# Optimization experiments

Hardware: AMD Instinct MI355X
Metric: run time of the kernel (lower is better)

Reference implementation:

```python
import jax, jax.numpy as jnp
import numpy as np

B, T, E, UNITS, VOCAB, NCLS = 128, 512, 256, 256, 50257, 2

def setup_inputs() -> dict:
    key = jax.random.key(0)
    ks = jax.random.split(key, 7)
    s = 0.05
    return {
        "sentence": jax.random.randint(ks[0], (B, T), 0, VOCAB, dtype=jnp.int32),
        "emb_table": jax.random.normal(ks[1], (VOCAB, E), jnp.float32) * s,
        "W": jax.random.normal(ks[2], (1, UNITS, E), jnp.float32) * s,
        "U": jax.random.normal(ks[3], (1, UNITS, UNITS), jnp.float32) * s,
        "W1": jax.random.normal(ks[4], (UNITS, 32), jnp.float32) * s,
        "b1": jnp.zeros((32,), jnp.float32),
        "W2": jax.random.normal(ks[5], (32, NCLS), jnp.float32) * s,
        "b2": jnp.zeros((NCLS,), jnp.float32),
    }

def reference(sentence, emb_table, W, U, W1, b1, W2, b2):
    # Embedding lookup: [B, T, E]
    emb = emb_table[sentence]
    # Precompute input projection for all timesteps in one batched GEMM:
    # x @ W[0].T for every t -> [T, B, units]
    xW = jnp.einsum('bte,ue->tbu', emb, W[0])
    Ut = U[0].T  # [units, units]

    def step(h, xw_t):
        h_new = jnp.tanh(xw_t + h @ Ut)
        return h_new, None

    h0 = jnp.zeros((sentence.shape[0], W.shape[1]), emb.dtype)
    h_final, _ = jax.lax.scan(step, h0, xW)

    # Classification head (dropout is identity at inference)
    hidden = jax.nn.relu(h_final @ W1 + b1)
    logits = hidden @ W2 + b2
    return jax.nn.softmax(logits, axis=-1)
```

## Files before the change

kernel.cpp:

```cpp
#include <hip/hip_runtime.h>
#include <stdint.h>

#define TT 512
#define NB 128
#define EM 256
#define UN 256

typedef float floatx4 __attribute__((ext_vector_type(4)));
typedef int v8i __attribute__((ext_vector_type(8)));

#define SCALE_Q 0x7B7B7B7BU
#define SCALE_A 0x7D7D7D7DU

#define BAR() asm volatile("s_waitcnt lgkmcnt(0)\n\ts_barrier" ::: "memory")

__device__ inline unsigned char f2fp8(float f) {
    int pk = __builtin_amdgcn_cvt_pk_fp8_f32(f, f, 0, false);
    return (unsigned char)(pk & 0xff);
}
__device__ inline float fp8dec(uint32_t word, int sel) {
#if defined(__has_builtin)
#if __has_builtin(__builtin_amdgcn_cvt_f32_fp8)
    return __builtin_amdgcn_cvt_f32_fp8(word >> (8 * sel), 0);
#else
    unsigned char b = (word >> (8 * sel)) & 0xff;
    int s = b >> 7, e = (b >> 3) & 15, m = b & 7;
    float v = e ? ldexpf((float)(8 + m), e - 10) : ldexpf((float)m, -9);
    return s ? -v : v;
#endif
#else
    unsigned char b = (word >> (8 * sel)) & 0xff;
    int s = b >> 7, e = (b >> 3) & 15, m = b & 7;
    float v = e ? ldexpf((float)(8 + m), e - 10) : ldexpf((float)m, -9);
    return s ? -v : v;
#endif
}

__global__ void k_pack(const float* __restrict__ W, const float* __restrict__ U,
                       unsigned char* __restrict__ wfrag8, unsigned char* __restrict__ ufrag8) {
    int bid = blockIdx.x;
    const float* src = (bid < 32) ? W : U;
    unsigned char* dstbase = (bid < 32) ? wfrag8 : ufrag8;
    int idx = (bid & 31) * 256 + threadIdx.x;
    int jg   = idx & 3;
    int lane = (idx >> 2) & 63;
    int tile = idx >> 8;
    int nt = tile & 15, kh = tile >> 4;
    int u  = nt * 16 + (lane & 15);
    int k0 = kh * 128 + (lane >> 4) * 32 + jg * 8;
    unsigned char* dst = dstbase + ((size_t)tile * 64 + lane) * 32 + jg * 8;
    #pragma unroll
    for (int j = 0; j < 8; j++) dst[j] = f2fp8(16.f * src[u * EM + k0 + j]);
}

__device__ inline void gemm_burst(const unsigned char* __restrict__ wfrag8,
                                  const float4* araw, unsigned char* dst,
                                  int w, int m, int kg, int lane)
{
    union { uint32_t d[8]; v8i v; } B[2];
    #pragma unroll
    for (int kh = 0; kh < 2; kh++) {
        #pragma unroll
        for (int d2 = 0; d2 < 8; d2++) {
            float4 f = araw[kh * 8 + d2];
            int pk = __builtin_amdgcn_cvt_pk_fp8_f32(16.f * f.x, 16.f * f.y, 0, false);
            pk     = __builtin_amdgcn_cvt_pk_fp8_f32(16.f * f.z, 16.f * f.w, pk, true);
            B[kh].d[d2] = (uint32_t)pk;
        }
    }
    const floatx4 zero4 = {0.f, 0.f, 0.f, 0.f};
    const int lsout = w * 16 + m;
    const int sw = (lsout & 7) << 3;
    #pragma unroll
    for (int ut = 0; ut < 16; ut++) {
        union { uint4 u4[2]; v8i v; } A0, A1;
        const uint4* p0 = (const uint4*)(wfrag8 + ((size_t)(ut)      * 64 + lane) * 32);
        const uint4* p1 = (const uint4*)(wfrag8 + ((size_t)(16 + ut) * 64 + lane) * 32);
        A0.u4[0] = p0[0]; A0.u4[1] = p0[1];
        A1.u4[0] = p1[0]; A1.u4[1] = p1[1];
        floatx4 acc = __builtin_amdgcn_mfma_scale_f32_16x16x128_f8f6f4(
                          A0.v, B[0].v, zero4, 0, 0, 0, SCALE_Q, 0, SCALE_Q);
        acc = __builtin_amdgcn_mfma_scale_f32_16x16x128_f8f6f4(
                          A1.v, B[1].v, acc, 0, 0, 0, SCALE_Q, 0, SCALE_Q);
        int pk = __builtin_amdgcn_cvt_pk_fp8_f32(16.f * acc[0], 16.f * acc[1], 0, false);
        pk     = __builtin_amdgcn_cvt_pk_fp8_f32(16.f * acc[2], 16.f * acc[3], pk, true);
        int wi = (ut * 4 + kg) ^ sw;
        *(uint32_t*)(dst + (size_t)lsout * 256 + wi * 4) = (uint32_t)pk;
    }
}

__global__ __launch_bounds__(256, 1) void k_rnn(
    const int* __restrict__ sent, const float* __restrict__ emb,
    const unsigned char* __restrict__ wfrag8, const unsigned char* __restrict__ ufrag8,
    const float* __restrict__ W1, const float* __restrict__ b1,
    const float* __restrict__ W2, const float* __restrict__ b2,
    float* __restrict__ out)
{
    __shared__ __align__(16) unsigned char hb8[2][256];
    __shared__ __align__(16) unsigned char xstage[2][64 * 256];
    __shared__ float hid[32];
    const int t    = threadIdx.x;
    const int lane = t & 63;
    const int w    = t >> 6;
    const int kg   = lane >> 4;
    const int m    = lane & 15;
    const int b    = blockIdx.x;

    v8i ufr8[4][2];
    #pragma unroll
    for (int q = 0; q < 4; q++) {
        #pragma unroll
        for (int kh = 0; kh < 2; kh++) {
            const uint4* p = (const uint4*)(ufrag8 + ((size_t)(kh * 16 + 4 * w + q) * 64 + lane) * 32);
            union { uint4 u4[2]; v8i v; } cvt;
            cvt.u4[0] = p[0]; cvt.u4[1] = p[1];
            ufr8[q][kh] = cvt.v;
        }
    }

    float4 araw[16];
    int tok = sent[b * TT + w * 16 + m];
    {
        const float* arow = emb + (size_t)tok * EM + kg * 32;
        #pragma unroll
        for (int kh = 0; kh < 2; kh++)
            #pragma unroll
            for (int d = 0; d < 8; d++)
                araw[kh * 8 + d] = *(const float4*)(arow + kh * 128 + 4 * d);
    }
    gemm_burst(wfrag8, araw, &xstage[0][0], w, m, kg, lane);

    hb8[0][t] = 0; hb8[1][t] = 0;
    __syncthreads();

    int hcur = 0, xcur = 0;
    const float c3 = -0.33333334f, c5 = 0.13333334f, c7 = -0.05396825f, c9 = 0.02186949f;
    const floatx4 zero4 = {0.f, 0.f, 0.f, 0.f};
    const int sel = lane >> 4;

    for (int s = 0; s < TT; s++) {
        const int ls = s & 63;
        int wi = (t >> 2) ^ ((ls & 7) << 3);
        uint32_t xword = *(const uint32_t*)&xstage[xcur][ls * 256 + wi * 4];
        float xf = fp8dec(xword, t & 3) * 0.0625f;

        const unsigned char* hc = hb8[hcur];
        union { uint4 u4[2]; v8i v; } A0, A1;
        A0.u4[0] = *(const uint4*)(hc + kg * 32);
        A0.u4[1] = *(const uint4*)(hc + kg * 32 + 16);
        A1.u4[0] = *(const uint4*)(hc + 128 + kg * 32);
        A1.u4[1] = *(const uint4*)(hc + 128 + kg * 32 + 16);

        float z[4];
        #pragma unroll
        for (int q = 0; q < 4; q++) {
            floatx4 acc = __builtin_amdgcn_mfma_scale_f32_16x16x128_f8f6f4(
                              A0.v, ufr8[q][0], zero4, 0, 0, 0, SCALE_A, 0, SCALE_Q);
            acc = __builtin_amdgcn_mfma_scale_f32_16x16x128_f8f6f4(
                              A1.v, ufr8[q][1], acc, 0, 0, 0, SCALE_A, 0, SCALE_Q);
            z[q] = acc[0];
        }

        float zz = (sel == 0) ? z[0] : (sel == 1) ? z[1] : (sel == 2) ? z[2] : z[3];
        zz += xf;

        float hn;
        if (__builtin_expect(fabsf(zz) > 0.75f, 0)) {
            float e = __expf(2.f * zz);
            hn = 1.f - 2.f * __builtin_amdgcn_rcpf(e + 1.f);
        } else {
            float x2f = zz * zz;
            float p = fmaf(x2f, c9, c7);
            p = fmaf(x2f, p, c5);
            p = fmaf(x2f, p, c3);
            hn = fmaf(zz * x2f, p, zz);
        }

        hb8[hcur ^ 1][t] = f2fp8(4.f * hn);

        int nbase = (s & ~63) + 64;
        if (nbase < TT) {
            if (ls == 12) {
                tok = sent[b * TT + nbase + w * 16 + m];
            }
            if (ls == 16) {
                const float* arow = emb + (size_t)tok * EM + kg * 32;
                #pragma unroll
                for (int kh = 0; kh < 2; kh++)
                    #pragma unroll
                    for (int d = 0; d < 8; d++)
                        araw[kh * 8 + d] = *(const float4*)(arow + kh * 128 + 4 * d);
            }
            if (ls == 24) {
                gemm_burst(wfrag8, araw, &xstage[xcur ^ 1][0], w, m, kg, lane);
            }
        }
        if (ls == 63) xcur ^= 1;
        BAR();
        hcur ^= 1;
    }

    if (t < 32) {
        float a = b1[t];
        for (int k = 0; k < 256; k++) {
            uint32_t wd = *(const uint32_t*)&hb8[hcur][k & ~3];
            a += 0.25f * fp8dec(wd, k & 3) * W1[k * 32 + t];
        }
        hid[t] = fmaxf(a, 0.f);
    }
    __syncthreads();
    if (t == 0) {
        float l0 = b2[0], l1 = b2[1];
        #pragma unroll
        for (int i = 0; i < 32; i++) {
            float hv = hid[i];
            l0 += hv * W2[2 * i];
            l1 += hv * W2[2 * i + 1];
        }
        float mx2 = fmaxf(l0, l1);
        float e0 = __expf(l0 - mx2), e1 = __expf(l1 - mx2);
        float inv = 1.f / (e0 + e1);
        out[2 * b]     = e0 * inv;
        out[2 * b + 1] = e1 * inv;
    }
}

extern "C" void kernel_launch(void* const* d_in, const int* in_sizes, int n_in,
                              void* d_out, int out_size, void* d_ws, size_t ws_size,
                              hipStream_t stream) {
    const int*   sent = (const int*)d_in[0];
    const float* emb  = (const float*)d_in[1];
    const float* W    = (const float*)d_in[2];
    const float* U    = (const float*)d_in[3];
    const float* W1   = (const float*)d_in[4];
    const float* b1   = (const float*)d_in[5];
    const float* W2   = (const float*)d_in[6];
    const float* b2   = (const float*)d_in[7];
    float* out = (float*)d_out;

    unsigned char* wfrag8 = (unsigned char*)d_ws;
    unsigned char* ufrag8 = wfrag8 + (size_t)UN * EM;

    k_pack<<<64, 256, 0, stream>>>(W, U, wfrag8, ufrag8);
    k_rnn<<<NB, 256, 0, stream>>>(sent, emb, wfrag8, ufrag8, W1, b1, W2, b2, out);
}
```

Baseline: 308.1 us.

## Spread next-chunk input projection across recurrence steps and parallelize head

Replaces the one-shot gemm_burst for the next 64-step input chunk with a pipeline spread over steps: token fetch, embedding load, fp8 conversion, then one MFMA output tile per step across 16 steps, with W fragments prefetched one step ahead. This is meant to remove the latency spike that the burst added to one step of the serial recurrence. The two chained MFMAs per recurrent step become independent and are summed afterwards, which shortens the dependency chain. The classifier's first layer is split across all 256 threads with a shared-memory reduction. In exchange it holds more registers live across the loop and adds branches to every step.

```diff
diff --git a/kernel.cpp b/kernel.cpp
--- a/kernel.cpp
+++ b/kernel.cpp
@@ -98,6 +98,7 @@
 {
     __shared__ __align__(16) unsigned char hb8[2][256];
     __shared__ __align__(16) unsigned char xstage[2][64 * 256];
+    __shared__ float partial[256];
     __shared__ float hid[32];
     const int t    = threadIdx.x;
     const int lane = t & 63;
@@ -118,25 +119,30 @@
         }
     }
 
-    float4 araw[16];
-    int tok = sent[b * TT + w * 16 + m];
     {
+        float4 araw[16];
+        int tok = sent[b * TT + w * 16 + m];
         const float* arow = emb + (size_t)tok * EM + kg * 32;
         #pragma unroll
         for (int kh = 0; kh < 2; kh++)
             #pragma unroll
             for (int d = 0; d < 8; d++)
                 araw[kh * 8 + d] = *(const float4*)(arow + kh * 128 + 4 * d);
-    }
-    gemm_burst(wfrag8, araw, &xstage[0][0], w, m, kg, lane);
+        gemm_burst(wfrag8, araw, &xstage[0][0], w, m, kg, lane);
+    }
 
     hb8[0][t] = 0; hb8[1][t] = 0;
     __syncthreads();
 
     int hcur = 0, xcur = 0;
+    int ntok = 0;
+    float4 araw[16];
+    union { uint32_t d[8]; v8i v; } Bf[2];
+    uint4 pa[4];
     const float c3 = -0.33333334f, c5 = 0.13333334f, c7 = -0.05396825f, c9 = 0.02186949f;
     const floatx4 zero4 = {0.f, 0.f, 0.f, 0.f};
     const int sel = lane >> 4;
+    const int sw = ((w * 16 + m) & 7) << 3;
 
     for (int s = 0; s < TT; s++) {
         const int ls = s & 63;
@@ -154,11 +160,11 @@
         float z[4];
         #pragma unroll
         for (int q = 0; q < 4; q++) {
-            floatx4 acc = __builtin_amdgcn_mfma_scale_f32_16x16x128_f8f6f4(
-                              A0.v, ufr8[q][0], zero4, 0, 0, 0, SCALE_A, 0, SCALE_Q);
-            acc = __builtin_amdgcn_mfma_scale_f32_16x16x128_f8f6f4(
-                              A1.v, ufr8[q][1], acc, 0, 0, 0, SCALE_A, 0, SCALE_Q);
-            z[q] = acc[0];
+            floatx4 a0 = __builtin_amdgcn_mfma_scale_f32_16x16x128_f8f6f4(
+                             A0.v, ufr8[q][0], zero4, 0, 0, 0, SCALE_A, 0, SCALE_Q);
+            floatx4 a1 = __builtin_amdgcn_mfma_scale_f32_16x16x128_f8f6f4(
+                             A1.v, ufr8[q][1], zero4, 0, 0, 0, SCALE_A, 0, SCALE_Q);
+            z[q] = a0[0] + a1[0];
         }
 
         float zz = (sel == 0) ? z[0] : (sel == 1) ? z[1] : (sel == 2) ? z[2] : z[3];
@@ -178,35 +184,73 @@
 
         hb8[hcur ^ 1][t] = f2fp8(4.f * hn);
 
-        int nbase = (s & ~63) + 64;
-        if (nbase < TT) {
-            if (ls == 12) {
-                tok = sent[b * TT + nbase + w * 16 + m];
-            }
-            if (ls == 16) {
-                const float* arow = emb + (size_t)tok * EM + kg * 32;
+        if (s < TT - 64) {
+            if (ls == 8)
+                ntok = sent[b * TT + (s & ~63) + 64 + w * 16 + m];
+            if (ls == 10) {
+                const float* arow = emb + (size_t)ntok * EM + kg * 32;
                 #pragma unroll
                 for (int kh = 0; kh < 2; kh++)
                     #pragma unroll
                     for (int d = 0; d < 8; d++)
                         araw[kh * 8 + d] = *(const float4*)(arow + kh * 128 + 4 * d);
             }
-            if (ls == 24) {
-                gemm_burst(wfrag8, araw, &xstage[xcur ^ 1][0], w, m, kg, lane);
-            }
-        }
+            if (ls == 12) {
+                #pragma unroll
+                for (int kh = 0; kh < 2; kh++)
+                    #pragma unroll
+                    for (int d2 = 0; d2 < 8; d2++) {
+                        float4 f = araw[kh * 8 + d2];
+                        int pk = __builtin_amdgcn_cvt_pk_fp8_f32(16.f * f.x, 16.f * f.y, 0, false);
+                        pk     = __builtin_amdgcn_cvt_pk_fp8_f32(16.f * f.z, 16.f * f.w, pk, true);
+                        Bf[kh].d[d2] = (uint32_t)pk;
+                    }
+            }
+            if ((unsigned)(ls - 16) < 16u) {
+                int ut = ls - 16;
+                union { uint4 u4[2]; v8i v; } TA0, TA1;
+                TA0.u4[0] = pa[0]; TA0.u4[1] = pa[1];
+                TA1.u4[0] = pa[2]; TA1.u4[1] = pa[3];
+                floatx4 acc = __builtin_amdgcn_mfma_scale_f32_16x16x128_f8f6f4(
+                                  TA0.v, Bf[0].v, zero4, 0, 0, 0, SCALE_Q, 0, SCALE_Q);
+                acc = __builtin_amdgcn_mfma_scale_f32_16x16x128_f8f6f4(
+                                  TA1.v, Bf[1].v, acc, 0, 0, 0, SCALE_Q, 0, SCALE_Q);
+                int pk = __builtin_amdgcn_cvt_pk_fp8_f32(16.f * acc[0], 16.f * acc[1], 0, false);
+                pk     = __builtin_amdgcn_cvt_pk_fp8_f32(16.f * acc[2], 16.f * acc[3], pk, true);
+                int wiw = (ut * 4 + kg) ^ sw;
+                *(uint32_t*)(&xstage[xcur ^ 1][0] + (size_t)(w * 16 + m) * 256 + wiw * 4) = (uint32_t)pk;
+            }
+            if ((unsigned)(ls - 15) < 16u) {
+                int ut2 = ls - 15;
+                const uint4* p0 = (const uint4*)(wfrag8 + ((size_t)(ut2)      * 64 + lane) * 32);
+                const uint4* p1 = (const uint4*)(wfrag8 + ((size_t)(16 + ut2) * 64 + lane) * 32);
+                pa[0] = p0[0]; pa[1] = p0[1];
+                pa[2] = p1[0]; pa[3] = p1[1];
+            }
+        }
+
         if (ls == 63) xcur ^= 1;
         BAR();
         hcur ^= 1;
     }
 
+    {
+        int col = t & 31, seg = t >> 5;
+        float a = 0.f;
+        #pragma unroll
+        for (int kk = 0; kk < 32; kk++) {
+            int k = seg * 32 + kk;
+            uint32_t wd = *(const uint32_t*)&hb8[hcur][k & ~3];
+            a += fp8dec(wd, k & 3) * W1[k * 32 + col];
+        }
+        partial[t] = a;
+    }
+    __syncthreads();
     if (t < 32) {
-        float a = b1[t];
-        for (int k = 0; k < 256; k++) {
-            uint32_t wd = *(const uint32_t*)&hb8[hcur][k & ~3];
-            a += 0.25f * fp8dec(wd, k & 3) * W1[k * 32 + t];
-        }
-        hid[t] = fmaxf(a, 0.f);
+        float acc = 0.f;
+        #pragma unroll
+        for (int i = 0; i < 8; i++) acc += partial[i * 32 + t];
+        hid[t] = fmaxf(fmaf(0.25f, acc, b1[t]), 0.f);
     }
     __syncthreads();
     if (t == 0) {
```

Measured after the change: 402.3 us. 1.31x slower.
